# Kernel tuning notes

Measured on AMD Instinct MI355X. Metric: run time of the kernel, lower is better.

## Reference

```python
import jax, jax.numpy as jnp
import numpy as np

CLAMP_MIN, CLAMP_MAX = 1e-7, 10.0


def _hyper_layer(H, edge_nodes, W, b, power):
    """One HyperTensorGraphConvolution forward.

    H:          [N, d] node signals
    edge_nodes: [E, k] int node indices per hyperedge (k-1 < num_sample, so
                the sampling branch of the original code never triggers and the
                aggregation is the full power-mean over the k-1 neighbors)
    """
    H = jnp.clip(H, CLAMP_MIN, CLAMP_MAX)          # torch.clamp_(H, ...)
    inv_p = 1.0 / power
    Hp = H ** power                                 # [N, d]
    gathered = Hp[edge_nodes]                       # [E, k, d]
    edge_sum = gathered.sum(axis=1, keepdims=True)  # [E, 1, d]
    k = edge_nodes.shape[1]
    # power-mean of the other (k-1) nodes in the hyperedge, per incidence
    contrib = ((edge_sum - gathered) / (k - 1)) ** inv_p   # [E, k, d]
    # new_signal = H.clone(); scatter-add contributions per (edge, node)
    d = H.shape[1]
    new_signal = H.at[edge_nodes.reshape(-1)].add(contrib.reshape(-1, d))
    # row-normalize (rowsum^-1, inf -> 0)
    rowsum = new_signal.sum(axis=1, keepdims=True)
    r_inv = jnp.where(rowsum != 0, 1.0 / rowsum, 0.0)
    AH = new_signal * r_inv
    return AH @ W + b


def setup_inputs() -> dict:
    key = jax.random.key(0)
    k_x, k_e, k_w1, k_b1, k_w2, k_b2 = jax.random.split(key, 6)
    N, d, E, k, c = 100000, 128, 25000, 32, 40
    x = jax.random.uniform(k_x, (N, d), dtype=jnp.float32)
    edge_nodes = jax.random.randint(k_e, (E, k), 0, N, dtype=jnp.int64)
    std1 = 1.0 / np.sqrt(16.0)
    W1 = jax.random.uniform(k_w1, (d, 16), jnp.float32, -std1, std1)
    b1 = jax.random.uniform(k_b1, (16,), jnp.float32, -std1, std1)
    std2 = 1.0 / np.sqrt(float(c))
    W2 = jax.random.uniform(k_w2, (16, c), jnp.float32, -std2, std2)
    b2 = jax.random.uniform(k_b2, (c,), jnp.float32, -std2, std2)
    return {"x": x, "edge_nodes": edge_nodes, "W1": W1, "b1": b1,
            "W2": W2, "b2": b2, "power": 2}


def reference(x, edge_nodes, W1, b1, W2, b2, power):
    H = jax.nn.relu(_hyper_layer(x, edge_nodes, W1, b1, float(power)))
    # dropout is identity at inference
    out = _hyper_layer(H, edge_nodes, W2, b2, float(power))
    return out
```

## Files before the change

### kernel.cpp

```cpp
#include <hip/hip_runtime.h>
#include <hip/hip_fp16.h>
#include <math.h>

#define CAP 64
#define D1 128
#define D2 16
#define C_OUT 40
#define K_EDGE 32
#define CLAMP_LO 1e-7f
#define CLAMP_HI 10.0f
#define SQRT_INV31 0.1796053020267749f

typedef unsigned short ushort_t;

__global__ __launch_bounds__(256) void k_setup(const float* __restrict__ x,
                                               __half2* __restrict__ Hp,
                                               const int* __restrict__ idx,
                                               int* __restrict__ deg,
                                               ushort_t* __restrict__ lst,
                                               const float* __restrict__ W1,
                                               float* __restrict__ W1t,
                                               __half2* __restrict__ S,
                                               float* __restrict__ S2,
                                               int n4, int total, int E) {
    int i = blockIdx.x * 256 + threadIdx.x;
    if (i < n4) {
        float4 v = ((const float4*)x)[i];
        v.x = fminf(fmaxf(v.x, CLAMP_LO), CLAMP_HI);
        v.y = fminf(fmaxf(v.y, CLAMP_LO), CLAMP_HI);
        v.z = fminf(fmaxf(v.z, CLAMP_LO), CLAMP_HI);
        v.w = fminf(fmaxf(v.w, CLAMP_LO), CLAMP_HI);
        Hp[2 * i]     = __floats2half2_rn(v.x * v.x, v.y * v.y);
        Hp[2 * i + 1] = __floats2half2_rn(v.z * v.z, v.w * v.w);
    }
    if (i < total) {
        int n = idx[i];
        int e = i >> 5;
        int pos = atomicAdd(&deg[n], 1);
        if (pos < CAP) lst[n * CAP + pos] = (ushort_t)e;
    }
    if (i < D1 * D2) W1t[(i & 15) * D1 + (i >> 4)] = W1[i];
    if (i < 64) S[(size_t)E * 64 + i] = __floats2half2_rn(0.0f, 0.0f);
    if (i < D2) S2[(size_t)E * D2 + i] = 0.0f;
}

__global__ __launch_bounds__(256) void k_edge_sum(const __half2* __restrict__ Hp,
                                                  const int* __restrict__ idx,
                                                  __half2* __restrict__ S, int E) {
    int w = threadIdx.x >> 6;
    int lane = threadIdx.x & 63;
    int eA = blockIdx.x * 8 + w * 2;
    int nid = idx[eA * K_EDGE + lane];
    float a0 = 0.0f, a1 = 0.0f, b0 = 0.0f, b1 = 0.0f;
#pragma unroll
    for (int j = 0; j < K_EDGE; j++) {
        int nA = __builtin_amdgcn_readlane(nid, j);
        int nB = __builtin_amdgcn_readlane(nid, 32 + j);
        __half2 hA = Hp[(size_t)nA * 64 + lane];
        __half2 hB = Hp[(size_t)nB * 64 + lane];
        a0 += __low2float(hA); a1 += __high2float(hA);
        b0 += __low2float(hB); b1 += __high2float(hB);
    }
    S[(size_t)eA * 64 + lane]       = __floats2half2_rn(a0, a1);
    S[(size_t)(eA + 1) * 64 + lane] = __floats2half2_rn(b0, b1);
}

__global__ __launch_bounds__(256) void k_node1(const __half2* __restrict__ Hp,
                                               const __half2* __restrict__ S,
                                               const int* __restrict__ deg,
                                               const ushort_t* __restrict__ lst,
                                               const float* __restrict__ W1t,
                                               const float* __restrict__ b1,
                                               float* __restrict__ Hp2, int N, int E) {
    int w = threadIdx.x >> 6;
    int lane = threadIdx.x & 63;
    int pair = blockIdx.x * 4 + w;
    int n0 = pair * 2, n1 = n0 + 1;
    int c = lane & 15, j = lane >> 4;

    int2 dg2 = ((const int2*)deg)[pair];
    int dg0 = min(dg2.x, CAP), dg1 = min(dg2.y, CAP);
    int sl = lane & 15;
    int nodesel = (lane < 16) ? n0 : n1;
    ushort_t idu = (lane < 32) ? lst[nodesel * CAP + sl] : (ushort_t)0;
    int dsel = (lane < 16) ? dg0 : dg1;
    int e_sel = (lane < 32 && sl < dsel) ? (int)idu : E;

    __half2 hph0 = Hp[(size_t)n0 * 64 + lane];
    __half2 hph1 = Hp[(size_t)n1 * 64 + lane];

    __half2 sv0[16], sv1[16];
#pragma unroll
    for (int t = 0; t < 16; t++) {
        int e = __builtin_amdgcn_readlane(e_sel, t);
        sv0[t] = S[(size_t)e * 64 + lane];
    }
#pragma unroll
    for (int t = 0; t < 16; t++) {
        int e = __builtin_amdgcn_readlane(e_sel, 16 + t);
        sv1[t] = S[(size_t)e * 64 + lane];
    }

    float hp00 = __low2float(hph0), hp01 = __high2float(hph0);
    float hp10 = __low2float(hph1), hp11 = __high2float(hph1);

    float a00 = 0.0f, a01 = 0.0f, a10 = 0.0f, a11 = 0.0f;
#pragma unroll
    for (int t = 0; t < 16; t++) {
        a00 += __builtin_amdgcn_sqrtf(fmaxf(__low2float(sv0[t])  - hp00, 0.0f));
        a01 += __builtin_amdgcn_sqrtf(fmaxf(__high2float(sv0[t]) - hp01, 0.0f));
    }
#pragma unroll
    for (int t = 0; t < 16; t++) {
        a10 += __builtin_amdgcn_sqrtf(fmaxf(__low2float(sv1[t])  - hp10, 0.0f));
        a11 += __builtin_amdgcn_sqrtf(fmaxf(__high2float(sv1[t]) - hp11, 0.0f));
    }
    for (int t = 16; t < dg0; t++) {
        int e = lst[n0 * CAP + t];
        __half2 sh = S[(size_t)e * 64 + lane];
        a00 += __builtin_amdgcn_sqrtf(fmaxf(__low2float(sh)  - hp00, 0.0f));
        a01 += __builtin_amdgcn_sqrtf(fmaxf(__high2float(sh) - hp01, 0.0f));
    }
    for (int t = 16; t < dg1; t++) {
        int e = lst[n1 * CAP + t];
        __half2 sh = S[(size_t)e * 64 + lane];
        a10 += __builtin_amdgcn_sqrtf(fmaxf(__low2float(sh)  - hp10, 0.0f));
        a11 += __builtin_amdgcn_sqrtf(fmaxf(__high2float(sh) - hp11, 0.0f));
    }

    float ns00 = __builtin_amdgcn_sqrtf(hp00) + a00 * SQRT_INV31;
    float ns01 = __builtin_amdgcn_sqrtf(hp01) + a01 * SQRT_INV31;
    float ns10 = __builtin_amdgcn_sqrtf(hp10) + a10 * SQRT_INV31;
    float ns11 = __builtin_amdgcn_sqrtf(hp11) + a11 * SQRT_INV31;

    __shared__ float AHs[4][2][D1];
    AHs[w][0][2 * lane]     = ns00;
    AHs[w][0][2 * lane + 1] = ns01;
    AHs[w][1][2 * lane]     = ns10;
    AHs[w][1][2 * lane + 1] = ns11;

    float v0 = ns00 + ns01, v1 = ns10 + ns11;
#pragma unroll
    for (int m = 1; m < 64; m <<= 1) {
        v0 += __shfl_xor(v0, m, 64);
        v1 += __shfl_xor(v1, m, 64);
    }
    float r0 = __builtin_amdgcn_rcpf(v0);
    float r1 = __builtin_amdgcn_rcpf(v1);

    __threadfence_block();

    const float4* a0p = (const float4*)(&AHs[w][0][j * 32]);
    const float4* a1p = (const float4*)(&AHs[w][1][j * 32]);
    const float4* w1p = (const float4*)(W1t + c * D1 + j * 32);
    float p0 = 0.0f, p1 = 0.0f;
#pragma unroll
    for (int tt = 0; tt < 8; tt++) {
        float4 wv = w1p[tt];
        float4 x0 = a0p[tt];
        float4 x1 = a1p[tt];
        p0 += x0.x * wv.x + x0.y * wv.y + x0.z * wv.z + x0.w * wv.w;
        p1 += x1.x * wv.x + x1.y * wv.y + x1.z * wv.z + x1.w * wv.w;
    }
    p0 += __shfl_xor(p0, 16, 64);
    p0 += __shfl_xor(p0, 32, 64);
    p1 += __shfl_xor(p1, 16, 64);
    p1 += __shfl_xor(p1, 32, 64);
    if (lane < D2) {
        float bb = b1[c];
        float o0 = bb + p0 * r0;
        float o1 = bb + p1 * r1;
        float cl0 = fminf(fmaxf(o0, CLAMP_LO), CLAMP_HI);
        float cl1 = fminf(fmaxf(o1, CLAMP_LO), CLAMP_HI);
        Hp2[(size_t)n0 * D2 + c] = cl0 * cl0;
        Hp2[(size_t)n1 * D2 + c] = cl1 * cl1;
    }
}

__global__ __launch_bounds__(256) void k_edge_sum2(const float* __restrict__ Hp2,
                                                   const int* __restrict__ idx,
                                                   float* __restrict__ S2, int E) {
    int e = blockIdx.x * 16 + (threadIdx.x >> 4);
    int col = threadIdx.x & 15;
    if (e >= E) return;
    float acc = 0.0f;
#pragma unroll
    for (int j = 0; j < K_EDGE; j++) {
        int n = idx[e * K_EDGE + j];
        acc += Hp2[(size_t)n * D2 + col];
    }
    S2[(size_t)e * D2 + col] = acc;
}

__global__ __launch_bounds__(256) void k_node2(const float* __restrict__ Hp2,
                                               const float* __restrict__ S2,
                                               const int* __restrict__ deg,
                                               const ushort_t* __restrict__ lst,
                                               const float* __restrict__ W2,
                                               const float* __restrict__ b2,
                                               float* __restrict__ out, int N, int E) {
    int w = threadIdx.x >> 6;
    int lane = threadIdx.x & 63;
    int pair = blockIdx.x * 4 + w;
    int n0 = pair * 2, n1 = n0 + 1;
    int col = lane & 15;
    int node = lane >> 5;
    int gg = (lane >> 4) & 1;
    int nn = node ? n1 : n0;

    int2 dg2 = ((const int2*)deg)[pair];
    int dg0 = min(dg2.x, CAP), dg1 = min(dg2.y, CAP);
    int sl = lane & 15;
    ushort_t idu = (lane < 32) ? lst[((lane < 16) ? n0 : n1) * CAP + sl] : (ushort_t)0;
    int dsel = (lane < 16) ? dg0 : dg1;
    int e_sel = (lane < 32 && sl < dsel) ? (int)idu : E;

    float hp = Hp2[(size_t)nn * D2 + col];
    int dgn = node ? dg1 : dg0;

    int ev[8];
#pragma unroll
    for (int t = 0; t < 8; t++) ev[t] = __shfl(e_sel, node * 16 + 2 * t + gg, 64);
    float sv[8];
#pragma unroll
    for (int t = 0; t < 8; t++) sv[t] = S2[(size_t)ev[t] * D2 + col];

    float acc = 0.0f;
#pragma unroll
    for (int t = 0; t < 8; t++)
        acc += __builtin_amdgcn_sqrtf(fmaxf(sv[t] - hp, 0.0f));
    for (int t = 16; t < dgn; t++) {
        int e = lst[nn * CAP + t];
        float s = S2[(size_t)e * D2 + col];
        if (gg == 0) acc += __builtin_amdgcn_sqrtf(fmaxf(s - hp, 0.0f));
    }
    acc += __shfl_xor(acc, 16, 64);
    float ns = __builtin_amdgcn_sqrtf(hp) + acc * SQRT_INV31;

    float v = ns;
#pragma unroll
    for (int m = 1; m < 16; m <<= 1) v += __shfl_xor(v, m, 64);
    float r = __builtin_amdgcn_rcpf(v);

    __shared__ float AHs[4][2][D2];
    if (gg == 0) AHs[w][node][col] = ns * r;
    __threadfence_block();

    if (lane < C_OUT) {
        float o0 = b2[lane], o1 = o0;
#pragma unroll
        for (int i = 0; i < D2; i++) {
            float wv = W2[i * C_OUT + lane];
            o0 += AHs[w][0][i] * wv;
            o1 += AHs[w][1][i] * wv;
        }
        out[(size_t)n0 * C_OUT + lane] = o0;
        out[(size_t)n1 * C_OUT + lane] = o1;
    }
}

extern "C" void kernel_launch(void* const* d_in, const int* in_sizes, int n_in,
                              void* d_out, int out_size, void* d_ws, size_t ws_size,
                              hipStream_t stream) {
    const float* x   = (const float*)d_in[0];
    const int*   idx = (const int*)d_in[1];
    const float* W1  = (const float*)d_in[2];
    const float* b1  = (const float*)d_in[3];
    const float* W2  = (const float*)d_in[4];
    const float* b2  = (const float*)d_in[5];
    float* out = (float*)d_out;

    int N = in_sizes[0] / D1;
    int E = in_sizes[1] / K_EDGE;

    __half2* Hp = (__half2*)d_ws;
    __half2* S  = Hp + (size_t)N * 64;
    float* Hp2  = (float*)(S + (size_t)(E + 1) * 64);
    float* S2   = Hp2 + (size_t)N * D2;
    float* W1t  = S2 + (size_t)(E + 1) * D2;
    int*   deg  = (int*)(W1t + D1 * D2);
    ushort_t* lst = (ushort_t*)(deg + N);

    int total = E * K_EDGE;
    int n4 = N * D1 / 4;

    (void)hipMemsetAsync(deg, 0, (size_t)N * sizeof(int), stream);
    k_setup<<<(n4 + 255) / 256, 256, 0, stream>>>(x, Hp, idx, deg, lst, W1, W1t,
                                                  S, S2, n4, total, E);
    k_edge_sum<<<E / 8, 256, 0, stream>>>(Hp, idx, S, E);
    k_node1<<<N / 8, 256, 0, stream>>>(Hp, S, deg, lst, W1t, b1, Hp2, N, E);
    k_edge_sum2<<<(E + 15) / 16, 256, 0, stream>>>(Hp2, idx, S2, E);
    k_node2<<<N / 8, 256, 0, stream>>>(Hp2, S2, deg, lst, W2, b2, out, N, E);
}
```

Before: 260.5 us.

## Widen gathers to 16B/8B vectors and skip unneeded edge loads by degree

k_edge_sum now has each wave handle four edges, with each lane loading a 16-byte vector of eight fp16 values per neighbor, so wider and fewer gather instructions are issued. k_node1 splits the wave into two halves, one per node, and has each lane read 8-byte h4v vectors. It also does the subtraction and max in packed fp16, and loads and processes edge slots 8-15 only when a node's degree needs them. k_node2 likewise gates its second group of S2 loads on degree. Doing the subtraction in fp16 before the sqrt may change rounding slightly, and when the branches diverge some latency hiding is lost.

After: 261.1 us. No clear change (+0.2%).

```diff
diff --git a/kernel.cpp b/kernel.cpp
--- a/kernel.cpp
+++ b/kernel.cpp
@@ -12,6 +12,9 @@
 #define SQRT_INV31 0.1796053020267749f
 
 typedef unsigned short ushort_t;
+typedef _Float16 h2v __attribute__((ext_vector_type(2)));
+typedef _Float16 h4v __attribute__((ext_vector_type(4)));
+typedef _Float16 h8v __attribute__((ext_vector_type(8)));
 
 __global__ __launch_bounds__(256) void k_setup(const float* __restrict__ x,
                                                __half2* __restrict__ Hp,
@@ -49,20 +52,36 @@
                                                   __half2* __restrict__ S, int E) {
     int w = threadIdx.x >> 6;
     int lane = threadIdx.x & 63;
-    int eA = blockIdx.x * 8 + w * 2;
-    int nid = idx[eA * K_EDGE + lane];
-    float a0 = 0.0f, a1 = 0.0f, b0 = 0.0f, b1 = 0.0f;
+    int eA = blockIdx.x * 16 + w * 4;
+    if (eA >= E) return;
+    int q = lane >> 4;
+    int m = lane & 15;
+    int nid0 = idx[eA * K_EDGE + lane];
+    int nid1 = idx[(eA + 2) * K_EDGE + lane];
+    float acc[8];
+#pragma unroll
+    for (int i = 0; i < 8; i++) acc[i] = 0.0f;
 #pragma unroll
     for (int j = 0; j < K_EDGE; j++) {
-        int nA = __builtin_amdgcn_readlane(nid, j);
-        int nB = __builtin_amdgcn_readlane(nid, 32 + j);
-        __half2 hA = Hp[(size_t)nA * 64 + lane];
-        __half2 hB = Hp[(size_t)nB * 64 + lane];
-        a0 += __low2float(hA); a1 += __high2float(hA);
-        b0 += __low2float(hB); b1 += __high2float(hB);
-    }
-    S[(size_t)eA * 64 + lane]       = __floats2half2_rn(a0, a1);
-    S[(size_t)(eA + 1) * 64 + lane] = __floats2half2_rn(b0, b1);
+        int nA = __builtin_amdgcn_readlane(nid0, j);
+        int nB = __builtin_amdgcn_readlane(nid0, 32 + j);
+        int nC = __builtin_amdgcn_readlane(nid1, j);
+        int nD = __builtin_amdgcn_readlane(nid1, 32 + j);
+        int nLo = (q & 1) ? nB : nA;
+        int nHi = (q & 1) ? nD : nC;
+        int n = (q & 2) ? nHi : nLo;
+        h8v h = ((const h8v*)Hp)[(size_t)n * 16 + m];
+#pragma unroll
+        for (int i = 0; i < 8; i++) acc[i] += (float)h[i];
+    }
+    __half2 oo[4];
+    oo[0] = __floats2half2_rn(acc[0], acc[1]);
+    oo[1] = __floats2half2_rn(acc[2], acc[3]);
+    oo[2] = __floats2half2_rn(acc[4], acc[5]);
+    oo[3] = __floats2half2_rn(acc[6], acc[7]);
+    uint4 st;
+    __builtin_memcpy(&st, oo, 16);
+    ((uint4*)S)[(size_t)(eA + q) * 16 + m] = st;
 }
 
 __global__ __launch_bounds__(256) void k_node1(const __half2* __restrict__ Hp,
@@ -77,6 +96,7 @@
     int pair = blockIdx.x * 4 + w;
     int n0 = pair * 2, n1 = n0 + 1;
     int c = lane & 15, j = lane >> 4;
+    int half = lane >> 5, ll = lane & 31;
 
     int2 dg2 = ((const int2*)deg)[pair];
     int dg0 = min(dg2.x, CAP), dg1 = min(dg2.y, CAP);
@@ -86,65 +106,81 @@
     int dsel = (lane < 16) ? dg0 : dg1;
     int e_sel = (lane < 32 && sl < dsel) ? (int)idu : E;
 
-    __half2 hph0 = Hp[(size_t)n0 * 64 + lane];
-    __half2 hph1 = Hp[(size_t)n1 * 64 + lane];
-
-    __half2 sv0[16], sv1[16];
-#pragma unroll
-    for (int t = 0; t < 16; t++) {
-        int e = __builtin_amdgcn_readlane(e_sel, t);
-        sv0[t] = S[(size_t)e * 64 + lane];
-    }
-#pragma unroll
-    for (int t = 0; t < 16; t++) {
-        int e = __builtin_amdgcn_readlane(e_sel, 16 + t);
-        sv1[t] = S[(size_t)e * 64 + lane];
-    }
-
-    float hp00 = __low2float(hph0), hp01 = __high2float(hph0);
-    float hp10 = __low2float(hph1), hp11 = __high2float(hph1);
-
-    float a00 = 0.0f, a01 = 0.0f, a10 = 0.0f, a11 = 0.0f;
-#pragma unroll
-    for (int t = 0; t < 16; t++) {
-        a00 += __builtin_amdgcn_sqrtf(fmaxf(__low2float(sv0[t])  - hp00, 0.0f));
-        a01 += __builtin_amdgcn_sqrtf(fmaxf(__high2float(sv0[t]) - hp01, 0.0f));
-    }
-#pragma unroll
-    for (int t = 0; t < 16; t++) {
-        a10 += __builtin_amdgcn_sqrtf(fmaxf(__low2float(sv1[t])  - hp10, 0.0f));
-        a11 += __builtin_amdgcn_sqrtf(fmaxf(__high2float(sv1[t]) - hp11, 0.0f));
-    }
-    for (int t = 16; t < dg0; t++) {
-        int e = lst[n0 * CAP + t];
-        __half2 sh = S[(size_t)e * 64 + lane];
-        a00 += __builtin_amdgcn_sqrtf(fmaxf(__low2float(sh)  - hp00, 0.0f));
-        a01 += __builtin_amdgcn_sqrtf(fmaxf(__high2float(sh) - hp01, 0.0f));
-    }
-    for (int t = 16; t < dg1; t++) {
-        int e = lst[n1 * CAP + t];
-        __half2 sh = S[(size_t)e * 64 + lane];
-        a10 += __builtin_amdgcn_sqrtf(fmaxf(__low2float(sh)  - hp10, 0.0f));
-        a11 += __builtin_amdgcn_sqrtf(fmaxf(__high2float(sh) - hp11, 0.0f));
-    }
-
-    float ns00 = __builtin_amdgcn_sqrtf(hp00) + a00 * SQRT_INV31;
-    float ns01 = __builtin_amdgcn_sqrtf(hp01) + a01 * SQRT_INV31;
-    float ns10 = __builtin_amdgcn_sqrtf(hp10) + a10 * SQRT_INV31;
-    float ns11 = __builtin_amdgcn_sqrtf(hp11) + a11 * SQRT_INV31;
+    int nown = half ? n1 : n0;
+    h4v hp4 = ((const h4v*)Hp)[(size_t)nown * 32 + ll];
+    const h4v z4 = {(_Float16)0.0f, (_Float16)0.0f, (_Float16)0.0f, (_Float16)0.0f};
+
+    int dmaxc = min(max(dg0, dg1), 16);
+    float a0 = 0.0f, a1 = 0.0f, a2 = 0.0f, a3 = 0.0f;
+
+    h4v sv[12];
+#pragma unroll
+    for (int t = 0; t < 12; t++) {
+        int eA = __builtin_amdgcn_readlane(e_sel, t);
+        int eB = __builtin_amdgcn_readlane(e_sel, 16 + t);
+        int e = half ? eB : eA;
+        sv[t] = ((const h4v*)S)[(size_t)e * 32 + ll];
+    }
+#pragma unroll
+    for (int t = 0; t < 8; t++) {
+        h4v d = __builtin_elementwise_max(sv[t] - hp4, z4);
+        a0 += __builtin_amdgcn_sqrtf((float)d[0]);
+        a1 += __builtin_amdgcn_sqrtf((float)d[1]);
+        a2 += __builtin_amdgcn_sqrtf((float)d[2]);
+        a3 += __builtin_amdgcn_sqrtf((float)d[3]);
+    }
+    if (dmaxc > 8) {
+#pragma unroll
+        for (int t = 8; t < 12; t++) {
+            h4v d = __builtin_elementwise_max(sv[t] - hp4, z4);
+            a0 += __builtin_amdgcn_sqrtf((float)d[0]);
+            a1 += __builtin_amdgcn_sqrtf((float)d[1]);
+            a2 += __builtin_amdgcn_sqrtf((float)d[2]);
+            a3 += __builtin_amdgcn_sqrtf((float)d[3]);
+        }
+        if (dmaxc > 12) {
+#pragma unroll
+            for (int t = 0; t < 4; t++) {
+                int eA = __builtin_amdgcn_readlane(e_sel, 12 + t);
+                int eB = __builtin_amdgcn_readlane(e_sel, 28 + t);
+                int e = half ? eB : eA;
+                h4v s = ((const h4v*)S)[(size_t)e * 32 + ll];
+                h4v d = __builtin_elementwise_max(s - hp4, z4);
+                a0 += __builtin_amdgcn_sqrtf((float)d[0]);
+                a1 += __builtin_amdgcn_sqrtf((float)d[1]);
+                a2 += __builtin_amdgcn_sqrtf((float)d[2]);
+                a3 += __builtin_amdgcn_sqrtf((float)d[3]);
+            }
+        }
+    }
+    int dgn = half ? dg1 : dg0;
+    for (int t = 16; t < dgn; t++) {
+        int e = lst[nown * CAP + t];
+        h4v s = ((const h4v*)S)[(size_t)e * 32 + ll];
+        h4v d = __builtin_elementwise_max(s - hp4, z4);
+        a0 += __builtin_amdgcn_sqrtf((float)d[0]);
+        a1 += __builtin_amdgcn_sqrtf((float)d[1]);
+        a2 += __builtin_amdgcn_sqrtf((float)d[2]);
+        a3 += __builtin_amdgcn_sqrtf((float)d[3]);
+    }
+
+    float h0 = (float)hp4[0], h1f = (float)hp4[1];
+    float h2 = (float)hp4[2], h3 = (float)hp4[3];
+    float ns0 = __builtin_amdgcn_sqrtf(h0)  + a0 * SQRT_INV31;
+    float ns1 = __builtin_amdgcn_sqrtf(h1f) + a1 * SQRT_INV31;
+    float ns2 = __builtin_amdgcn_sqrtf(h2)  + a2 * SQRT_INV31;
+    float ns3 = __builtin_amdgcn_sqrtf(h3)  + a3 * SQRT_INV31;
 
     __shared__ float AHs[4][2][D1];
-    AHs[w][0][2 * lane]     = ns00;
-    AHs[w][0][2 * lane + 1] = ns01;
-    AHs[w][1][2 * lane]     = ns10;
-    AHs[w][1][2 * lane + 1] = ns11;
-
-    float v0 = ns00 + ns01, v1 = ns10 + ns11;
-#pragma unroll
-    for (int m = 1; m < 64; m <<= 1) {
-        v0 += __shfl_xor(v0, m, 64);
-        v1 += __shfl_xor(v1, m, 64);
-    }
+    float4 nsv = make_float4(ns0, ns1, ns2, ns3);
+    ((float4*)AHs[w][half])[ll] = nsv;
+
+    float v = ns0 + ns1 + ns2 + ns3;
+#pragma unroll
+    for (int m2 = 1; m2 < 32; m2 <<= 1) v += __shfl_xor(v, m2, 64);
+    float vO = __shfl_xor(v, 32, 64);
+    float v0 = half ? vO : v;
+    float v1 = half ? v : vO;
     float r0 = __builtin_amdgcn_rcpf(v0);
     float r1 = __builtin_amdgcn_rcpf(v1);
 
@@ -217,18 +253,31 @@
 
     float hp = Hp2[(size_t)nn * D2 + col];
     int dgn = node ? dg1 : dg0;
-
-    int ev[8];
-#pragma unroll
-    for (int t = 0; t < 8; t++) ev[t] = __shfl(e_sel, node * 16 + 2 * t + gg, 64);
-    float sv[8];
-#pragma unroll
-    for (int t = 0; t < 8; t++) sv[t] = S2[(size_t)ev[t] * D2 + col];
+    int dm = max(dg0, dg1);
 
     float acc = 0.0f;
-#pragma unroll
-    for (int t = 0; t < 8; t++)
-        acc += __builtin_amdgcn_sqrtf(fmaxf(sv[t] - hp, 0.0f));
+    {
+        int ev[4];
+#pragma unroll
+        for (int t = 0; t < 4; t++) ev[t] = __shfl(e_sel, node * 16 + 2 * t + gg, 64);
+        float sv[4];
+#pragma unroll
+        for (int t = 0; t < 4; t++) sv[t] = S2[(size_t)ev[t] * D2 + col];
+#pragma unroll
+        for (int t = 0; t < 4; t++)
+            acc += __builtin_amdgcn_sqrtf(fmaxf(sv[t] - hp, 0.0f));
+    }
+    if (dm > 8) {
+        int ev[4];
+#pragma unroll
+        for (int t = 0; t < 4; t++) ev[t] = __shfl(e_sel, node * 16 + 2 * (4 + t) + gg, 64);
+        float sv[4];
+#pragma unroll
+        for (int t = 0; t < 4; t++) sv[t] = S2[(size_t)ev[t] * D2 + col];
+#pragma unroll
+        for (int t = 0; t < 4; t++)
+            acc += __builtin_amdgcn_sqrtf(fmaxf(sv[t] - hp, 0.0f));
+    }
     for (int t = 16; t < dgn; t++) {
         int e = lst[nn * CAP + t];
         float s = S2[(size_t)e * D2 + col];
@@ -287,7 +336,7 @@
     (void)hipMemsetAsync(deg, 0, (size_t)N * sizeof(int), stream);
     k_setup<<<(n4 + 255) / 256, 256, 0, stream>>>(x, Hp, idx, deg, lst, W1, W1t,
                                                   S, S2, n4, total, E);
-    k_edge_sum<<<E / 8, 256, 0, stream>>>(Hp, idx, S, E);
+    k_edge_sum<<<(E + 15) / 16, 256, 0, stream>>>(Hp, idx, S, E);
     k_node1<<<N / 8, 256, 0, stream>>>(Hp, S, deg, lst, W1t, b1, Hp2, N, E);
     k_edge_sum2<<<(E + 15) / 16, 256, 0, stream>>>(Hp2, idx, S2, E);
     k_node2<<<N / 8, 256, 0, stream>>>(Hp2, S2, deg, lst, W2, b2, out, N, E);
```

## Process four nodes per wave in node1 with packed fp16 and degree-gated loops

Applied to the files above, without the earlier changes.

k_node1 now handles four nodes per wavefront instead of two. The first 12 edge sums per node are prefetched, and the max(S - Hp, 0) step uses packed half2 arithmetic before the float sqrt. The later 8..16 incidence iterations are skipped when no node in the wave has that many edges, and Hp2 is written with one coalesced 64-lane store. k_node2 gets a similar degree gate on its upper half of the unrolled loop. The aim is to cut wasted work on padded or out-of-range slots (average degree is about 8) and per-node overhead. In exchange, register pressure rises and subtraction now happens in fp16 precision.

New measurement: 247.0 us. 1.05x faster.

```diff
diff --git a/kernel.cpp b/kernel.cpp
--- a/kernel.cpp
+++ b/kernel.cpp
@@ -12,6 +12,7 @@
 #define SQRT_INV31 0.1796053020267749f
 
 typedef unsigned short ushort_t;
+typedef _Float16 h2v __attribute__((ext_vector_type(2)));
 
 __global__ __launch_bounds__(256) void k_setup(const float* __restrict__ x,
                                                __half2* __restrict__ Hp,
@@ -74,107 +75,204 @@
                                                float* __restrict__ Hp2, int N, int E) {
     int w = threadIdx.x >> 6;
     int lane = threadIdx.x & 63;
-    int pair = blockIdx.x * 4 + w;
-    int n0 = pair * 2, n1 = n0 + 1;
+    int quad = blockIdx.x * 4 + w;
+    int n0 = quad * 4;
     int c = lane & 15, j = lane >> 4;
-
-    int2 dg2 = ((const int2*)deg)[pair];
-    int dg0 = min(dg2.x, CAP), dg1 = min(dg2.y, CAP);
-    int sl = lane & 15;
-    int nodesel = (lane < 16) ? n0 : n1;
-    ushort_t idu = (lane < 32) ? lst[nodesel * CAP + sl] : (ushort_t)0;
-    int dsel = (lane < 16) ? dg0 : dg1;
-    int e_sel = (lane < 32 && sl < dsel) ? (int)idu : E;
-
-    __half2 hph0 = Hp[(size_t)n0 * 64 + lane];
-    __half2 hph1 = Hp[(size_t)n1 * 64 + lane];
-
-    __half2 sv0[16], sv1[16];
-#pragma unroll
-    for (int t = 0; t < 16; t++) {
-        int e = __builtin_amdgcn_readlane(e_sel, t);
-        sv0[t] = S[(size_t)e * 64 + lane];
-    }
-#pragma unroll
-    for (int t = 0; t < 16; t++) {
-        int e = __builtin_amdgcn_readlane(e_sel, 16 + t);
-        sv1[t] = S[(size_t)e * 64 + lane];
-    }
-
-    float hp00 = __low2float(hph0), hp01 = __high2float(hph0);
-    float hp10 = __low2float(hph1), hp11 = __high2float(hph1);
-
-    float a00 = 0.0f, a01 = 0.0f, a10 = 0.0f, a11 = 0.0f;
-#pragma unroll
-    for (int t = 0; t < 16; t++) {
-        a00 += __builtin_amdgcn_sqrtf(fmaxf(__low2float(sv0[t])  - hp00, 0.0f));
-        a01 += __builtin_amdgcn_sqrtf(fmaxf(__high2float(sv0[t]) - hp01, 0.0f));
-    }
-#pragma unroll
-    for (int t = 0; t < 16; t++) {
-        a10 += __builtin_amdgcn_sqrtf(fmaxf(__low2float(sv1[t])  - hp10, 0.0f));
-        a11 += __builtin_amdgcn_sqrtf(fmaxf(__high2float(sv1[t]) - hp11, 0.0f));
-    }
-    for (int t = 16; t < dg0; t++) {
-        int e = lst[n0 * CAP + t];
-        __half2 sh = S[(size_t)e * 64 + lane];
-        a00 += __builtin_amdgcn_sqrtf(fmaxf(__low2float(sh)  - hp00, 0.0f));
-        a01 += __builtin_amdgcn_sqrtf(fmaxf(__high2float(sh) - hp01, 0.0f));
-    }
-    for (int t = 16; t < dg1; t++) {
-        int e = lst[n1 * CAP + t];
-        __half2 sh = S[(size_t)e * 64 + lane];
-        a10 += __builtin_amdgcn_sqrtf(fmaxf(__low2float(sh)  - hp10, 0.0f));
-        a11 += __builtin_amdgcn_sqrtf(fmaxf(__high2float(sh) - hp11, 0.0f));
-    }
-
-    float ns00 = __builtin_amdgcn_sqrtf(hp00) + a00 * SQRT_INV31;
-    float ns01 = __builtin_amdgcn_sqrtf(hp01) + a01 * SQRT_INV31;
-    float ns10 = __builtin_amdgcn_sqrtf(hp10) + a10 * SQRT_INV31;
-    float ns11 = __builtin_amdgcn_sqrtf(hp11) + a11 * SQRT_INV31;
-
-    __shared__ float AHs[4][2][D1];
-    AHs[w][0][2 * lane]     = ns00;
-    AHs[w][0][2 * lane + 1] = ns01;
-    AHs[w][1][2 * lane]     = ns10;
-    AHs[w][1][2 * lane + 1] = ns11;
-
-    float v0 = ns00 + ns01, v1 = ns10 + ns11;
+    int sl = lane & 15, g = lane >> 4;
+
+    int4 d4 = ((const int4*)deg)[quad];
+    int dgA = min(d4.x, CAP), dgB = min(d4.y, CAP);
+    int dgC = min(d4.z, CAP), dgD = min(d4.w, CAP);
+
+    ushort_t idu = lst[(n0 + g) * CAP + sl];
+    int dsel = (g == 0) ? dgA : (g == 1) ? dgB : (g == 2) ? dgC : dgD;
+    int e_sel = (sl < dsel) ? (int)idu : E;
+
+    __half2 hphA = Hp[(size_t)(n0 + 0) * 64 + lane];
+    __half2 hphB = Hp[(size_t)(n0 + 1) * 64 + lane];
+    __half2 hphC = Hp[(size_t)(n0 + 2) * 64 + lane];
+    __half2 hphD = Hp[(size_t)(n0 + 3) * 64 + lane];
+    h2v hpA, hpB, hpC, hpD;
+    __builtin_memcpy(&hpA, &hphA, 4);
+    __builtin_memcpy(&hpB, &hphB, 4);
+    __builtin_memcpy(&hpC, &hphC, 4);
+    __builtin_memcpy(&hpD, &hphD, 4);
+    const h2v zv = (h2v)(_Float16)0.0f;
+
+    int dmax = max(max(dgA, dgB), max(dgC, dgD));
+    int dmaxc = min(dmax, 16);
+
+    float aA0 = 0.0f, aA1 = 0.0f, aB0 = 0.0f, aB1 = 0.0f;
+    float aC0 = 0.0f, aC1 = 0.0f, aD0 = 0.0f, aD1 = 0.0f;
+
+    h2v sA[12], sB[12], sC[12], sD[12];
+#pragma unroll
+    for (int t = 0; t < 12; t++) {
+        int eA = __builtin_amdgcn_readlane(e_sel, t);
+        int eB = __builtin_amdgcn_readlane(e_sel, 16 + t);
+        int eC = __builtin_amdgcn_readlane(e_sel, 32 + t);
+        int eD = __builtin_amdgcn_readlane(e_sel, 48 + t);
+        __half2 hv;
+        hv = S[(size_t)eA * 64 + lane]; __builtin_memcpy(&sA[t], &hv, 4);
+        hv = S[(size_t)eB * 64 + lane]; __builtin_memcpy(&sB[t], &hv, 4);
+        hv = S[(size_t)eC * 64 + lane]; __builtin_memcpy(&sC[t], &hv, 4);
+        hv = S[(size_t)eD * 64 + lane]; __builtin_memcpy(&sD[t], &hv, 4);
+    }
+
+#pragma unroll
+    for (int t = 0; t < 8; t++) {
+        h2v dA = __builtin_elementwise_max(sA[t] - hpA, zv);
+        h2v dB = __builtin_elementwise_max(sB[t] - hpB, zv);
+        h2v dC = __builtin_elementwise_max(sC[t] - hpC, zv);
+        h2v dD = __builtin_elementwise_max(sD[t] - hpD, zv);
+        aA0 += __builtin_amdgcn_sqrtf((float)dA[0]);
+        aA1 += __builtin_amdgcn_sqrtf((float)dA[1]);
+        aB0 += __builtin_amdgcn_sqrtf((float)dB[0]);
+        aB1 += __builtin_amdgcn_sqrtf((float)dB[1]);
+        aC0 += __builtin_amdgcn_sqrtf((float)dC[0]);
+        aC1 += __builtin_amdgcn_sqrtf((float)dC[1]);
+        aD0 += __builtin_amdgcn_sqrtf((float)dD[0]);
+        aD1 += __builtin_amdgcn_sqrtf((float)dD[1]);
+    }
+
+    if (dmaxc > 8) {
+#pragma unroll
+        for (int t = 8; t < 12; t++) {
+            h2v dA = __builtin_elementwise_max(sA[t] - hpA, zv);
+            h2v dB = __builtin_elementwise_max(sB[t] - hpB, zv);
+            h2v dC = __builtin_elementwise_max(sC[t] - hpC, zv);
+            h2v dD = __builtin_elementwise_max(sD[t] - hpD, zv);
+            aA0 += __builtin_amdgcn_sqrtf((float)dA[0]);
+            aA1 += __builtin_amdgcn_sqrtf((float)dA[1]);
+            aB0 += __builtin_amdgcn_sqrtf((float)dB[0]);
+            aB1 += __builtin_amdgcn_sqrtf((float)dB[1]);
+            aC0 += __builtin_amdgcn_sqrtf((float)dC[0]);
+            aC1 += __builtin_amdgcn_sqrtf((float)dC[1]);
+            aD0 += __builtin_amdgcn_sqrtf((float)dD[0]);
+            aD1 += __builtin_amdgcn_sqrtf((float)dD[1]);
+        }
+        if (dmaxc > 12) {
+#pragma unroll
+            for (int t = 0; t < 4; t++) {
+                int eA = __builtin_amdgcn_readlane(e_sel, 12 + t);
+                int eB = __builtin_amdgcn_readlane(e_sel, 28 + t);
+                int eC = __builtin_amdgcn_readlane(e_sel, 44 + t);
+                int eD = __builtin_amdgcn_readlane(e_sel, 60 + t);
+                __half2 hv;
+                h2v uA, uB, uC, uD;
+                hv = S[(size_t)eA * 64 + lane]; __builtin_memcpy(&uA, &hv, 4);
+                hv = S[(size_t)eB * 64 + lane]; __builtin_memcpy(&uB, &hv, 4);
+                hv = S[(size_t)eC * 64 + lane]; __builtin_memcpy(&uC, &hv, 4);
+                hv = S[(size_t)eD * 64 + lane]; __builtin_memcpy(&uD, &hv, 4);
+                h2v dA = __builtin_elementwise_max(uA - hpA, zv);
+                h2v dB = __builtin_elementwise_max(uB - hpB, zv);
+                h2v dC = __builtin_elementwise_max(uC - hpC, zv);
+                h2v dD = __builtin_elementwise_max(uD - hpD, zv);
+                aA0 += __builtin_amdgcn_sqrtf((float)dA[0]);
+                aA1 += __builtin_amdgcn_sqrtf((float)dA[1]);
+                aB0 += __builtin_amdgcn_sqrtf((float)dB[0]);
+                aB1 += __builtin_amdgcn_sqrtf((float)dB[1]);
+                aC0 += __builtin_amdgcn_sqrtf((float)dC[0]);
+                aC1 += __builtin_amdgcn_sqrtf((float)dC[1]);
+                aD0 += __builtin_amdgcn_sqrtf((float)dD[0]);
+                aD1 += __builtin_amdgcn_sqrtf((float)dD[1]);
+            }
+        }
+    }
+
+    if (dmax > 16) {
+        float hA0 = (float)hpA[0], hA1 = (float)hpA[1];
+        float hB0 = (float)hpB[0], hB1 = (float)hpB[1];
+        float hC0 = (float)hpC[0], hC1 = (float)hpC[1];
+        float hD0 = (float)hpD[0], hD1 = (float)hpD[1];
+        for (int t = 16; t < dgA; t++) {
+            int e = lst[(n0 + 0) * CAP + t];
+            __half2 sh = S[(size_t)e * 64 + lane];
+            aA0 += __builtin_amdgcn_sqrtf(fmaxf(__low2float(sh)  - hA0, 0.0f));
+            aA1 += __builtin_amdgcn_sqrtf(fmaxf(__high2float(sh) - hA1, 0.0f));
+        }
+        for (int t = 16; t < dgB; t++) {
+            int e = lst[(n0 + 1) * CAP + t];
+            __half2 sh = S[(size_t)e * 64 + lane];
+            aB0 += __builtin_amdgcn_sqrtf(fmaxf(__low2float(sh)  - hB0, 0.0f));
+            aB1 += __builtin_amdgcn_sqrtf(fmaxf(__high2float(sh) - hB1, 0.0f));
+        }
+        for (int t = 16; t < dgC; t++) {
+            int e = lst[(n0 + 2) * CAP + t];
+            __half2 sh = S[(size_t)e * 64 + lane];
+            aC0 += __builtin_amdgcn_sqrtf(fmaxf(__low2float(sh)  - hC0, 0.0f));
+            aC1 += __builtin_amdgcn_sqrtf(fmaxf(__high2float(sh) - hC1, 0.0f));
+        }
+        for (int t = 16; t < dgD; t++) {
+            int e = lst[(n0 + 3) * CAP + t];
+            __half2 sh = S[(size_t)e * 64 + lane];
+            aD0 += __builtin_amdgcn_sqrtf(fmaxf(__low2float(sh)  - hD0, 0.0f));
+            aD1 += __builtin_amdgcn_sqrtf(fmaxf(__high2float(sh) - hD1, 0.0f));
+        }
+    }
+
+    float nsA0 = __builtin_amdgcn_sqrtf((float)hpA[0]) + aA0 * SQRT_INV31;
+    float nsA1 = __builtin_amdgcn_sqrtf((float)hpA[1]) + aA1 * SQRT_INV31;
+    float nsB0 = __builtin_amdgcn_sqrtf((float)hpB[0]) + aB0 * SQRT_INV31;
+    float nsB1 = __builtin_amdgcn_sqrtf((float)hpB[1]) + aB1 * SQRT_INV31;
+    float nsC0 = __builtin_amdgcn_sqrtf((float)hpC[0]) + aC0 * SQRT_INV31;
+    float nsC1 = __builtin_amdgcn_sqrtf((float)hpC[1]) + aC1 * SQRT_INV31;
+    float nsD0 = __builtin_amdgcn_sqrtf((float)hpD[0]) + aD0 * SQRT_INV31;
+    float nsD1 = __builtin_amdgcn_sqrtf((float)hpD[1]) + aD1 * SQRT_INV31;
+
+    __shared__ float AHs[4][4][D1];
+    AHs[w][0][2 * lane] = nsA0;  AHs[w][0][2 * lane + 1] = nsA1;
+    AHs[w][1][2 * lane] = nsB0;  AHs[w][1][2 * lane + 1] = nsB1;
+    AHs[w][2][2 * lane] = nsC0;  AHs[w][2][2 * lane + 1] = nsC1;
+    AHs[w][3][2 * lane] = nsD0;  AHs[w][3][2 * lane + 1] = nsD1;
+
+    float vA = nsA0 + nsA1, vB = nsB0 + nsB1;
+    float vC = nsC0 + nsC1, vD = nsD0 + nsD1;
 #pragma unroll
     for (int m = 1; m < 64; m <<= 1) {
-        v0 += __shfl_xor(v0, m, 64);
-        v1 += __shfl_xor(v1, m, 64);
-    }
-    float r0 = __builtin_amdgcn_rcpf(v0);
-    float r1 = __builtin_amdgcn_rcpf(v1);
+        vA += __shfl_xor(vA, m, 64);
+        vB += __shfl_xor(vB, m, 64);
+        vC += __shfl_xor(vC, m, 64);
+        vD += __shfl_xor(vD, m, 64);
+    }
+    float rA = __builtin_amdgcn_rcpf(vA);
+    float rB = __builtin_amdgcn_rcpf(vB);
+    float rC = __builtin_amdgcn_rcpf(vC);
+    float rD = __builtin_amdgcn_rcpf(vD);
 
     __threadfence_block();
 
-    const float4* a0p = (const float4*)(&AHs[w][0][j * 32]);
-    const float4* a1p = (const float4*)(&AHs[w][1][j * 32]);
+    const float4* aAp = (const float4*)(&AHs[w][0][j * 32]);
+    const float4* aBp = (const float4*)(&AHs[w][1][j * 32]);
+    const float4* aCp = (const float4*)(&AHs[w][2][j * 32]);
+    const float4* aDp = (const float4*)(&AHs[w][3][j * 32]);
     const float4* w1p = (const float4*)(W1t + c * D1 + j * 32);
-    float p0 = 0.0f, p1 = 0.0f;
+    float pA = 0.0f, pB = 0.0f, pC = 0.0f, pD = 0.0f;
 #pragma unroll
     for (int tt = 0; tt < 8; tt++) {
         float4 wv = w1p[tt];
-        float4 x0 = a0p[tt];
-        float4 x1 = a1p[tt];
-        p0 += x0.x * wv.x + x0.y * wv.y + x0.z * wv.z + x0.w * wv.w;
-        p1 += x1.x * wv.x + x1.y * wv.y + x1.z * wv.z + x1.w * wv.w;
-    }
-    p0 += __shfl_xor(p0, 16, 64);
-    p0 += __shfl_xor(p0, 32, 64);
-    p1 += __shfl_xor(p1, 16, 64);
-    p1 += __shfl_xor(p1, 32, 64);
-    if (lane < D2) {
-        float bb = b1[c];
-        float o0 = bb + p0 * r0;
-        float o1 = bb + p1 * r1;
-        float cl0 = fminf(fmaxf(o0, CLAMP_LO), CLAMP_HI);
-        float cl1 = fminf(fmaxf(o1, CLAMP_LO), CLAMP_HI);
-        Hp2[(size_t)n0 * D2 + c] = cl0 * cl0;
-        Hp2[(size_t)n1 * D2 + c] = cl1 * cl1;
-    }
+        float4 xA = aAp[tt];
+        float4 xB = aBp[tt];
+        float4 xC = aCp[tt];
+        float4 xD = aDp[tt];
+        pA += xA.x * wv.x + xA.y * wv.y + xA.z * wv.z + xA.w * wv.w;
+        pB += xB.x * wv.x + xB.y * wv.y + xB.z * wv.z + xB.w * wv.w;
+        pC += xC.x * wv.x + xC.y * wv.y + xC.z * wv.z + xC.w * wv.w;
+        pD += xD.x * wv.x + xD.y * wv.y + xD.z * wv.z + xD.w * wv.w;
+    }
+    pA += __shfl_xor(pA, 16, 64);  pA += __shfl_xor(pA, 32, 64);
+    pB += __shfl_xor(pB, 16, 64);  pB += __shfl_xor(pB, 32, 64);
+    pC += __shfl_xor(pC, 16, 64);  pC += __shfl_xor(pC, 32, 64);
+    pD += __shfl_xor(pD, 16, 64);  pD += __shfl_xor(pD, 32, 64);
+
+    float bb = b1[c];
+    float oA = fminf(fmaxf(bb + pA * rA, CLAMP_LO), CLAMP_HI);
+    float oB = fminf(fmaxf(bb + pB * rB, CLAMP_LO), CLAMP_HI);
+    float oC = fminf(fmaxf(bb + pC * rC, CLAMP_LO), CLAMP_HI);
+    float oD = fminf(fmaxf(bb + pD * rD, CLAMP_LO), CLAMP_HI);
+    float qA = oA * oA, qB = oB * oB, qC = oC * oC, qD = oD * oD;
+    float val = (g == 0) ? qA : (g == 1) ? qB : (g == 2) ? qC : qD;
+    Hp2[(size_t)quad * 64 + lane] = val;
 }
 
 __global__ __launch_bounds__(256) void k_edge_sum2(const float* __restrict__ Hp2,
@@ -217,6 +315,7 @@
 
     float hp = Hp2[(size_t)nn * D2 + col];
     int dgn = node ? dg1 : dg0;
+    int dm = max(dg0, dg1);
 
     int ev[8];
 #pragma unroll
@@ -227,8 +326,13 @@
 
     float acc = 0.0f;
 #pragma unroll
-    for (int t = 0; t < 8; t++)
+    for (int t = 0; t < 4; t++)
         acc += __builtin_amdgcn_sqrtf(fmaxf(sv[t] - hp, 0.0f));
+    if (dm > 8) {
+#pragma unroll
+        for (int t = 4; t < 8; t++)
+            acc += __builtin_amdgcn_sqrtf(fmaxf(sv[t] - hp, 0.0f));
+    }
     for (int t = 16; t < dgn; t++) {
         int e = lst[nn * CAP + t];
         float s = S2[(size_t)e * D2 + col];
@@ -288,7 +392,7 @@
     k_setup<<<(n4 + 255) / 256, 256, 0, stream>>>(x, Hp, idx, deg, lst, W1, W1t,
                                                   S, S2, n4, total, E);
     k_edge_sum<<<E / 8, 256, 0, stream>>>(Hp, idx, S, E);
-    k_node1<<<N / 8, 256, 0, stream>>>(Hp, S, deg, lst, W1t, b1, Hp2, N, E);
+    k_node1<<<N / 16, 256, 0, stream>>>(Hp, S, deg, lst, W1t, b1, Hp2, N, E);
     k_edge_sum2<<<(E + 15) / 16, 256, 0, stream>>>(Hp2, idx, S2, E);
     k_node2<<<N / 8, 256, 0, stream>>>(Hp2, S2, deg, lst, W2, b2, out, N, E);
 }
```
